# Optimization experiments

Hardware: AMD Instinct MI355X
Metric: run time of the kernel (lower is better)

## Reference

```python
import math
import jax, jax.numpy as jnp
import numpy as np

B, C, H, W = 8, 64, 128, 128
KH = KW = 3
PAD = 1
STRIDE = 1
DIL = 1
GROUPS = 4


def setup_inputs() -> dict:
    key = jax.random.key(0)
    k1, k2, k3, k4, k5 = jax.random.split(key, 5)
    x = jax.random.normal(k1, (B, C, H, W), jnp.float32)
    skip = jax.random.normal(k2, (B, C, H, W), jnp.float32)
    # offset-predicting conv: in_channels -> 2*KH*KW (has bias). Small init so offsets are modest.
    offset_w = jax.random.normal(k3, (2 * KH * KW, C, KH, KW), jnp.float32) * 0.01
    offset_b = jax.random.normal(k4, (2 * KH * KW,), jnp.float32) * 0.01
    # deformable conv weight: grouped, no bias. [Cout, Cin//G, KH, KW]
    fan_in = (C // GROUPS) * KH * KW
    deform_w = jax.random.normal(k5, (C, C // GROUPS, KH, KW), jnp.float32) * (1.0 / math.sqrt(fan_in))
    return {"x": x, "skip": skip, "offset_w": offset_w, "offset_b": offset_b, "deform_w": deform_w}


def _conv2d(x, w, b):
    y = jax.lax.conv_general_dilated(
        x, w, window_strides=(STRIDE, STRIDE), padding=((PAD, PAD), (PAD, PAD)),
        rhs_dilation=(DIL, DIL), dimension_numbers=("NCHW", "OIHW", "NCHW"))
    return y + b[None, :, None, None]


def _deform_conv(skip, offsets, w):
    # torchvision DeformConv2d semantics, offset_groups=1, zero-padded bilinear sampling.
    Bn, Cn, Hn, Wn = skip.shape
    Ho, Wo = offsets.shape[2], offsets.shape[3]
    K = KH * KW
    # offsets: [B, 2*K, Ho, Wo] ordered (k, (dy, dx))
    off = offsets.reshape(Bn, K, 2, Ho, Wo)
    off_y, off_x = off[:, :, 0], off[:, :, 1]  # [B,K,Ho,Wo]
    ky, kx = jnp.meshgrid(jnp.arange(KH), jnp.arange(KW), indexing="ij")
    ky, kx = ky.reshape(K), kx.reshape(K)
    base_y = (jnp.arange(Ho) * STRIDE - PAD)[None, None, :, None] + (ky * DIL)[None, :, None, None]
    base_x = (jnp.arange(Wo) * STRIDE - PAD)[None, None, None, :] + (kx * DIL)[None, :, None, None]
    py = base_y + off_y  # [B,K,Ho,Wo] sampling rows
    px = base_x + off_x  # sampling cols
    y0f = jnp.floor(py)
    x0f = jnp.floor(px)
    wy = py - y0f
    wx = px - x0f
    y0 = y0f.astype(jnp.int32)
    x0 = x0f.astype(jnp.int32)
    skip_flat = skip.reshape(Bn, Cn, Hn * Wn)

    def gather(yi, xi):
        valid = ((yi >= 0) & (yi < Hn) & (xi >= 0) & (xi < Wn)).astype(skip.dtype)  # [B,K,Ho,Wo]
        idx = jnp.clip(yi, 0, Hn - 1) * Wn + jnp.clip(xi, 0, Wn - 1)
        v = jax.vmap(lambda f, i: f[:, i])(skip_flat, idx.reshape(Bn, -1))  # [B,C,K*Ho*Wo]
        return v.reshape(Bn, Cn, K, Ho, Wo) * valid[:, None]

    v00 = gather(y0, x0)
    v01 = gather(y0, x0 + 1)
    v10 = gather(y0 + 1, x0)
    v11 = gather(y0 + 1, x0 + 1)
    wy_b = wy[:, None]  # [B,1,K,Ho,Wo]
    wx_b = wx[:, None]
    sampled = (v00 * (1 - wy_b) * (1 - wx_b) + v01 * (1 - wy_b) * wx_b
               + v10 * wy_b * (1 - wx_b) + v11 * wy_b * wx_b)  # [B,C,K,Ho,Wo]
    # grouped contraction with the kernel weights
    G = GROUPS
    Cg = Cn // G
    Cout = w.shape[0]
    Cog = Cout // G
    sampled_g = sampled.reshape(Bn, G, Cg, K, Ho, Wo)
    w_g = w.reshape(G, Cog, Cg, K)
    out = jnp.einsum("bgckhw,gock->bgohw", sampled_g, w_g)
    return out.reshape(Bn, Cout, Ho, Wo)


def reference(x, skip, offset_w, offset_b, deform_w):
    offsets = _conv2d(x, offset_w, offset_b)
    return _deform_conv(skip, offsets, deform_w)
```

## Files before the change

### kernel.cpp

```cpp
#include <hip/hip_runtime.h>
#include <hip/hip_fp16.h>

#define Bn    8
#define Cn    64
#define Hn    128
#define Wn    128
#define KK    9
#define OffC  18
#define NG    4
#define Cg    16
#define HW    (Hn*Wn)

#define OFFS_ELEMS (Bn*OffC*HW)
#define WAO_ELEMS  (KK*4*64*8)
#define WAD_ELEMS  (NG*KK*64*8)

#define ROWS  4
#define TR    8
#define NW    8
#define TSTR  132
#define TILE_W (NW*TR*TSTR)
#define TILE_PAD (TSTR + 4)

typedef __attribute__((ext_vector_type(8)))  short short8v;
typedef __attribute__((ext_vector_type(8)))  _Float16 half8v;
typedef __attribute__((ext_vector_type(4)))  unsigned int uint4v;
typedef __attribute__((ext_vector_type(16))) float f32x16;

__device__ __forceinline__ unsigned int rne16(float f) {
    unsigned int u = __float_as_uint(f);
    return (u + 0x7FFFu + ((u >> 16) & 1u)) >> 16;
}
__device__ __forceinline__ unsigned int pack2(float lo, float hi) {
    const unsigned int a = rne16(lo);
    unsigned int b = __float_as_uint(hi);
    b = (b + 0x7FFFu + ((b >> 16) & 1u)) & 0xFFFF0000u;
    return b | a;
}

__global__ __launch_bounds__(256) void prep_w_kernel(
    const float* __restrict__ offw, const float* __restrict__ dw,
    unsigned short* __restrict__ wAo, unsigned short* __restrict__ wAd)
{
    const int tid = blockIdx.x * 256 + threadIdx.x;
    const int nth = gridDim.x * 256;
    for (int i = tid; i < WAO_ELEMS; i += nth) {
        const int e    = i & 7;
        const int lane = (i >> 3) & 63;
        const int q    = (i >> 9) & 3;
        const int t    = i >> 11;
        const int o    = lane & 31;
        const int c    = q * 16 + 8 * (lane >> 5) + e;
        const float v  = (o < OffC) ? offw[(o * Cn + c) * KK + t] : 0.f;
        wAo[i] = (unsigned short)rne16(v);
    }
    for (int i = tid; i < WAD_ELEMS; i += nth) {
        const int e    = i & 7;
        const int lane = (i >> 3) & 63;
        const int t    = (i >> 9) % KK;
        const int g    = i / (512 * KK);
        const int o    = lane & 31;
        const int c    = 8 * (lane >> 5) + e;
        const float v  = (o < Cg) ? dw[((g * Cg + o) * Cg + c) * KK + t] : 0.f;
        wAd[i] = __half_as_ushort(__float2half_rn(v));
    }
}

__global__ __launch_bounds__(256, 4) void offset_conv_kernel(
    const float* __restrict__ x, const unsigned short* __restrict__ wAo,
    const float* __restrict__ bias, float2* __restrict__ offs2)
{
    const int tid  = threadIdx.x;
    const int wv   = tid >> 6;
    const int lane = tid & 63;
    const int p    = lane & 31;
    const int h    = lane >> 5;
    const int b    = blockIdx.y;
    const int r    = blockIdx.x;
    const int col  = wv * 32 + p;

    const float* xb = x + (size_t)b * Cn * HW;

    f32x16 acc;
#pragma unroll
    for (int i = 0; i < 16; ++i) acc[i] = 0.f;

#pragma unroll 1
    for (int q = 0; q < 4; ++q) {
        unsigned int win[4][3][3];
#pragma unroll
        for (int i = 0; i < 4; ++i) {
            const float* xc0 = xb + (size_t)(q * 16 + 8 * h + 2 * i) * HW;
            const float* xc1 = xc0 + HW;
#pragma unroll
            for (int ky = 0; ky < 3; ++ky) {
                const int  y   = r - 1 + ky;
                const bool yok = ((unsigned)y < (unsigned)Hn);
#pragma unroll
                for (int kx = 0; kx < 3; ++kx) {
                    const int  xx = col - 1 + kx;
                    const bool ok = yok && ((unsigned)xx < (unsigned)Wn);
                    const float f0 = ok ? xc0[y * Wn + xx] : 0.f;
                    const float f1 = ok ? xc1[y * Wn + xx] : 0.f;
                    win[i][ky][kx] = pack2(f0, f1);
                }
            }
        }
#pragma unroll
        for (int t = 0; t < KK; ++t) {
            uint4v bw;
            bw[0] = win[0][t / 3][t % 3];
            bw[1] = win[1][t / 3][t % 3];
            bw[2] = win[2][t / 3][t % 3];
            bw[3] = win[3][t / 3][t % 3];
            const short8v bfrag = __builtin_bit_cast(short8v, bw);
            const short8v afrag = *(const short8v*)(wAo + (size_t)(t * 4 + q) * 512 + lane * 8);
            acc = __builtin_amdgcn_mfma_f32_32x32x16_bf16(afrag, bfrag, acc, 0, 0, 0);
        }
    }

    float2* ob2 = offs2 + ((size_t)b * KK) * HW + r * Wn + col;
#pragma unroll
    for (int reg = 0; reg < 16; reg += 2) {
        const int o = (reg & 3) + 8 * (reg >> 2) + 4 * h;
        if (o < OffC) {
            const int t = o >> 1;
            float2 v;
            v.x = acc[reg]     + bias[o];
            v.y = acc[reg + 1] + bias[o + 1];
            ob2[(size_t)t * HW] = v;
        }
    }
}

struct TapS {
    int   base;
    int   gr0, gr1, gc0, gc1;
    float m00, m01, m10, m11;
    bool  cond;
};

__device__ __forceinline__ TapS tap_setup(
    int r, int col, int ky, int kx, float offy, float offx, int ylo, int yhi)
{
    TapS s;
    const float pyf = (float)(r - 1 + ky) + offy;
    const float pxf = (float)(col - 1 + kx) + offx;
    const float y0f = floorf(pyf), x0f = floorf(pxf);
    const float wy = pyf - y0f, wx = pxf - x0f;
    const int y0 = (int)y0f, x0 = (int)x0f;
    const int by = min(max(y0, 0), Hn - 1);
    const int bx = min(max(x0, 0), Wn - 1);
    const float w0p = (by == y0) ? (1.f - wy) : ((by == y0 + 1) ? wy : 0.f);
    const float w1p = (by == y0 && y0 + 1 <= Hn - 1) ? wy : 0.f;
    const float v0p = (bx == x0) ? (1.f - wx) : ((bx == x0 + 1) ? wx : 0.f);
    const float v1p = (bx == x0 && x0 + 1 <= Wn - 1) ? wx : 0.f;
    s.m00 = w0p * v0p; s.m01 = w0p * v1p;
    s.m10 = w1p * v0p; s.m11 = w1p * v1p;
    s.base = (by - ylo) * TSTR + bx;
    s.cond = (by >= ylo) && (min(by + 1, Hn - 1) <= yhi);
    s.gr0 = by; s.gr1 = min(by + 1, Hn - 1);
    s.gc0 = bx; s.gc1 = min(bx + 1, Wn - 1);
    return s;
}

__device__ __forceinline__ uint4v tap_sample(
    const TapS& s, int h, const __half2* __restrict__ tile,
    const float* __restrict__ sg)
{
    uint4v bw;
    if (s.cond) {
        const __half2 m00h = __float2half2_rn(s.m00);
        const __half2 m01h = __float2half2_rn(s.m01);
        const __half2 m10h = __float2half2_rn(s.m10);
        const __half2 m11h = __float2half2_rn(s.m11);
#pragma unroll
        for (int wi = 0; wi < 4; ++wi) {
            const __half2* tw = tile + ((4 * h + wi) * TR) * TSTR;
            __half2 a = __hmul2(tw[s.base], m00h);
            a = __hfma2(tw[s.base + 1], m01h, a);
            a = __hfma2(tw[s.base + TSTR], m10h, a);
            a = __hfma2(tw[s.base + TSTR + 1], m11h, a);
            bw[wi] = __builtin_bit_cast(unsigned int, a);
        }
    } else {
        const int ia0 = s.gr0 * Wn + s.gc0, ia1 = s.gr0 * Wn + s.gc1;
        const int ia2 = s.gr1 * Wn + s.gc0, ia3 = s.gr1 * Wn + s.gc1;
#pragma unroll
        for (int wi = 0; wi < 4; ++wi) {
            const float* sc0 = sg + (size_t)(8 * h + 2 * wi) * HW;
            const float* sc1 = sc0 + HW;
            const float v0 = sc0[ia0] * s.m00 + sc0[ia1] * s.m01 + sc0[ia2] * s.m10 + sc0[ia3] * s.m11;
            const float v1 = sc1[ia0] * s.m00 + sc1[ia1] * s.m01 + sc1[ia2] * s.m10 + sc1[ia3] * s.m11;
            bw[wi] = __builtin_bit_cast(unsigned int, __floats2half2_rn(v0, v1));
        }
    }
    return bw;
}

__device__ __forceinline__ uint4v chunk_tap(
    int r, int col, int ky, int kx, float oy, float ox, int ylo, int yhi, int h,
    const __half2* __restrict__ tile, const float* __restrict__ sg)
{
    const float pyf = (float)(r - 1 + ky) + oy;
    const float pxf = (float)(col - 1 + kx) + ox;
    const float y0f = floorf(pyf), x0f = floorf(pxf);
    const float wy = pyf - y0f, wx = pxf - x0f;
    const int y0 = (int)y0f, x0 = (int)x0f;
    const bool interior = (y0 >= ylo) & (y0 + 1 <= yhi) & (x0 >= 0) & (x0 + 1 <= Wn - 1);

    uint4v bw;
    if (__all(interior)) {
        const float iy = 1.f - wy, ix = 1.f - wx;
        const __half2 m00h = __float2half2_rn(iy * ix);
        const __half2 m01h = __float2half2_rn(iy * wx);
        const __half2 m10h = __float2half2_rn(wy * ix);
        const __half2 m11h = __float2half2_rn(wy * wx);
        const int base = (y0 - ylo) * TSTR + x0;
#pragma unroll
        for (int wi = 0; wi < 4; ++wi) {
            const __half2* tw = tile + ((4 * h + wi) * TR) * TSTR;
            __half2 a = __hmul2(tw[base], m00h);
            a = __hfma2(tw[base + 1], m01h, a);
            a = __hfma2(tw[base + TSTR], m10h, a);
            a = __hfma2(tw[base + TSTR + 1], m11h, a);
            bw[wi] = __builtin_bit_cast(unsigned int, a);
        }
    } else {
        const TapS s = tap_setup(r, col, ky, kx, oy, ox, ylo, yhi);
        bw = tap_sample(s, h, tile, sg);
    }
    return bw;
}

__global__ __launch_bounds__(512, 4) void deform_kernel(
    const float* __restrict__ skip, const float2* __restrict__ offs2,
    const unsigned short* __restrict__ wA, float* __restrict__ out)
{
    __shared__ __half2 tile[TILE_W + TILE_PAD];

    const int tid = threadIdx.x;
    const int g = blockIdx.y & 3;
    const int b = blockIdx.y >> 2;
    const int r0  = blockIdx.x * ROWS;
    const int ylo = max(0, r0 - 2);
    const int yhi = min(Hn - 1, r0 + ROWS + 1);

    const float* sg = skip + (size_t)(b * Cn + g * Cg) * HW;

    for (int i = tid; i < TILE_W; i += 512) {
        const int w  = i / (TR * TSTR);
        const int re = i % (TR * TSTR);
        const int ty = re / TSTR;
        const int xx = re % TSTR;
        const int y  = ylo + ty;
        __half2 v = __floats2half2_rn(0.f, 0.f);
        if (xx < Wn && y <= yhi) {
            const float f0 = sg[(2 * w)     * HW + y * Wn + xx];
            const float f1 = sg[(2 * w + 1) * HW + y * Wn + xx];
            v = __floats2half2_rn(f0, f1);
        }
        tile[i] = v;
    }
    for (int i = TILE_W + tid; i < TILE_W + TILE_PAD; i += 512)
        tile[i] = __floats2half2_rn(0.f, 0.f);
    __syncthreads();

    const int wv   = tid >> 6;
    const int lane = tid & 63;
    const int p    = lane & 31;
    const int h    = lane >> 5;
    const int r    = r0 + (wv >> 1);
    const int jb   = (wv & 1) * 2;
    const int colA = jb * 32 + p;
    const int colB = colA + 32;

    const unsigned short* wAg = wA + (size_t)g * (KK * 512) + lane * 8;
    const float2* offpA = offs2 + (size_t)b * KK * HW + r * Wn + colA;
    const float2* offpB = offpA + 32;

    f32x16 accA, accB;
#pragma unroll
    for (int i = 0; i < 16; ++i) { accA[i] = 0.f; accB[i] = 0.f; }

#pragma unroll
    for (int t = 0; t < KK; ++t) {
        const int ky = t / 3, kx = t % 3;
        const float2 oA = offpA[(size_t)t * HW];
        const float2 oB = offpB[(size_t)t * HW];

        const uint4v bwA = chunk_tap(r, colA, ky, kx, oA.x, oA.y, ylo, yhi, h, tile, sg);
        const uint4v bwB = chunk_tap(r, colB, ky, kx, oB.x, oB.y, ylo, yhi, h, tile, sg);

        const half8v afrag = *(const half8v*)(wAg + t * 512);
        accA = __builtin_amdgcn_mfma_f32_32x32x16_f16(afrag, __builtin_bit_cast(half8v, bwA), accA, 0, 0, 0);
        accB = __builtin_amdgcn_mfma_f32_32x32x16_f16(afrag, __builtin_bit_cast(half8v, bwB), accB, 0, 0, 0);
    }

    float* obA = out + (size_t)(b * Cn + g * Cg) * HW + r * Wn + colA;
#pragma unroll
    for (int reg = 0; reg < 8; ++reg) {
        const int o = (reg & 3) + 8 * (reg >> 2) + 4 * h;
        obA[o * HW]      = accA[reg];
        obA[o * HW + 32] = accB[reg];
    }
}

extern "C" void kernel_launch(void* const* d_in, const int* in_sizes, int n_in,
                              void* d_out, int out_size, void* d_ws, size_t ws_size,
                              hipStream_t stream) {
    const float* x        = (const float*)d_in[0];
    const float* skip     = (const float*)d_in[1];
    const float* offset_w = (const float*)d_in[2];
    const float* offset_b = (const float*)d_in[3];
    const float* deform_w = (const float*)d_in[4];
    float* out  = (float*)d_out;

    float2* offs2 = (float2*)d_ws;
    unsigned short* wAo = (unsigned short*)((float*)d_ws + OFFS_ELEMS);
    unsigned short* wAd = wAo + WAO_ELEMS;

    hipLaunchKernelGGL(prep_w_kernel, dim3(8), dim3(256), 0, stream,
                       offset_w, deform_w, wAo, wAd);
    hipLaunchKernelGGL(offset_conv_kernel, dim3(Hn, Bn), dim3(256), 0, stream,
                       x, wAo, offset_b, offs2);
    hipLaunchKernelGGL(deform_kernel, dim3(Hn / ROWS, Bn * NG), dim3(512), 0, stream,
                       skip, offs2, wAd, out);
}
```

Measured before the change: 75.78 us.

## Split deform conv tile into half-width column blocks with halo

Splits each block's work along the width into two 64-column halves. Each block now stages a 68-column tile with a halo instead of the full 128-wide row, and runs 256 threads instead of 512. The number of blocks doubles and shared memory per block roughly halves, which should raise occupancy and reduce tile-load latency. In exchange the halo columns are loaded twice, and the global-memory fallback path triggers more often near the column seams when offsets reach outside the narrower tile.

```diff
diff --git a/kernel.cpp b/kernel.cpp
--- a/kernel.cpp
+++ b/kernel.cpp
@@ -17,10 +17,11 @@
 
 #define ROWS  4
 #define TR    8
-#define NW    8
-#define TSTR  132
-#define TILE_W (NW*TR*TSTR)
-#define TILE_PAD (TSTR + 4)
+#define XT    68
+#define TSTRX 70
+#define PLANE (TR*TSTRX)
+#define TILE_WX (8*PLANE)
+#define TILE_PADX 72
 
 typedef __attribute__((ext_vector_type(8)))  short short8v;
 typedef __attribute__((ext_vector_type(8)))  _Float16 half8v;
@@ -141,7 +142,8 @@
 };
 
 __device__ __forceinline__ TapS tap_setup(
-    int r, int col, int ky, int kx, float offy, float offx, int ylo, int yhi)
+    int r, int col, int ky, int kx, float offy, float offx,
+    int ylo, int yhi, int xlo0, int xloR, int xhiR)
 {
     TapS s;
     const float pyf = (float)(r - 1 + ky) + offy;
@@ -157,8 +159,9 @@
     const float v1p = (bx == x0 && x0 + 1 <= Wn - 1) ? wx : 0.f;
     s.m00 = w0p * v0p; s.m01 = w0p * v1p;
     s.m10 = w1p * v0p; s.m11 = w1p * v1p;
-    s.base = (by - ylo) * TSTR + bx;
-    s.cond = (by >= ylo) && (min(by + 1, Hn - 1) <= yhi);
+    s.base = (by - ylo) * TSTRX + (bx - xlo0);
+    s.cond = (by >= ylo) && (min(by + 1, Hn - 1) <= yhi)
+          && (bx >= xloR) && (min(bx + 1, Wn - 1) <= xhiR);
     s.gr0 = by; s.gr1 = min(by + 1, Hn - 1);
     s.gc0 = bx; s.gc1 = min(bx + 1, Wn - 1);
     return s;
@@ -176,11 +179,11 @@
         const __half2 m11h = __float2half2_rn(s.m11);
 #pragma unroll
         for (int wi = 0; wi < 4; ++wi) {
-            const __half2* tw = tile + ((4 * h + wi) * TR) * TSTR;
+            const __half2* tw = tile + (4 * h + wi) * PLANE;
             __half2 a = __hmul2(tw[s.base], m00h);
             a = __hfma2(tw[s.base + 1], m01h, a);
-            a = __hfma2(tw[s.base + TSTR], m10h, a);
-            a = __hfma2(tw[s.base + TSTR + 1], m11h, a);
+            a = __hfma2(tw[s.base + TSTRX], m10h, a);
+            a = __hfma2(tw[s.base + TSTRX + 1], m11h, a);
             bw[wi] = __builtin_bit_cast(unsigned int, a);
         }
     } else {
@@ -199,7 +202,8 @@
 }
 
 __device__ __forceinline__ uint4v chunk_tap(
-    int r, int col, int ky, int kx, float oy, float ox, int ylo, int yhi, int h,
+    int r, int col, int ky, int kx, float oy, float ox,
+    int ylo, int yhi, int xlo0, int xloR, int xhiR, int h,
     const __half2* __restrict__ tile, const float* __restrict__ sg)
 {
     const float pyf = (float)(r - 1 + ky) + oy;
@@ -207,7 +211,7 @@
     const float y0f = floorf(pyf), x0f = floorf(pxf);
     const float wy = pyf - y0f, wx = pxf - x0f;
     const int y0 = (int)y0f, x0 = (int)x0f;
-    const bool interior = (y0 >= ylo) & (y0 + 1 <= yhi) & (x0 >= 0) & (x0 + 1 <= Wn - 1);
+    const bool interior = (y0 >= ylo) & (y0 + 1 <= yhi) & (x0 >= xloR) & (x0 + 1 <= xhiR);
 
     uint4v bw;
     if (__all(interior)) {
@@ -216,53 +220,60 @@
         const __half2 m01h = __float2half2_rn(iy * wx);
         const __half2 m10h = __float2half2_rn(wy * ix);
         const __half2 m11h = __float2half2_rn(wy * wx);
-        const int base = (y0 - ylo) * TSTR + x0;
+        const int base = (y0 - ylo) * TSTRX + (x0 - xlo0);
 #pragma unroll
         for (int wi = 0; wi < 4; ++wi) {
-            const __half2* tw = tile + ((4 * h + wi) * TR) * TSTR;
+            const __half2* tw = tile + (4 * h + wi) * PLANE;
             __half2 a = __hmul2(tw[base], m00h);
             a = __hfma2(tw[base + 1], m01h, a);
-            a = __hfma2(tw[base + TSTR], m10h, a);
-            a = __hfma2(tw[base + TSTR + 1], m11h, a);
+            a = __hfma2(tw[base + TSTRX], m10h, a);
+            a = __hfma2(tw[base + TSTRX + 1], m11h, a);
             bw[wi] = __builtin_bit_cast(unsigned int, a);
         }
     } else {
-        const TapS s = tap_setup(r, col, ky, kx, oy, ox, ylo, yhi);
+        const TapS s = tap_setup(r, col, ky, kx, oy, ox, ylo, yhi, xlo0, xloR, xhiR);
         bw = tap_sample(s, h, tile, sg);
     }
     return bw;
 }
 
-__global__ __launch_bounds__(512, 4) void deform_kernel(
+__global__ __launch_bounds__(256, 8) void deform_kernel(
     const float* __restrict__ skip, const float2* __restrict__ offs2,
     const unsigned short* __restrict__ wA, float* __restrict__ out)
 {
-    __shared__ __half2 tile[TILE_W + TILE_PAD];
+    __shared__ __half2 tile[TILE_WX + TILE_PADX];
 
     const int tid = threadIdx.x;
-    const int g = blockIdx.y & 3;
-    const int b = blockIdx.y >> 2;
+    const int yb  = blockIdx.y;
+    const int xh  = yb & 1;
+    const int g   = (yb >> 1) & 3;
+    const int b   = yb >> 3;
     const int r0  = blockIdx.x * ROWS;
     const int ylo = max(0, r0 - 2);
     const int yhi = min(Hn - 1, r0 + ROWS + 1);
+    const int xb  = xh * 64;
+    const int xlo0 = xb - 2;
+    const int xloR = max(0, xlo0);
+    const int xhiR = min(Wn - 1, xb + 65);
 
     const float* sg = skip + (size_t)(b * Cn + g * Cg) * HW;
 
-    for (int i = tid; i < TILE_W; i += 512) {
-        const int w  = i / (TR * TSTR);
-        const int re = i % (TR * TSTR);
-        const int ty = re / TSTR;
-        const int xx = re % TSTR;
+    for (int i = tid; i < TILE_WX; i += 256) {
+        const int w  = i / PLANE;
+        const int re = i % PLANE;
+        const int ty = re / TSTRX;
+        const int j  = re % TSTRX;
         const int y  = ylo + ty;
+        const int x  = xlo0 + j;
         __half2 v = __floats2half2_rn(0.f, 0.f);
-        if (xx < Wn && y <= yhi) {
-            const float f0 = sg[(2 * w)     * HW + y * Wn + xx];
-            const float f1 = sg[(2 * w + 1) * HW + y * Wn + xx];
+        if (j < XT && y <= yhi && x >= 0 && x < Wn) {
+            const float f0 = sg[(2 * w)     * HW + y * Wn + x];
+            const float f1 = sg[(2 * w + 1) * HW + y * Wn + x];
             v = __floats2half2_rn(f0, f1);
         }
         tile[i] = v;
     }
-    for (int i = TILE_W + tid; i < TILE_W + TILE_PAD; i += 512)
+    for (int i = TILE_WX + tid; i < TILE_WX + TILE_PADX; i += 256)
         tile[i] = __floats2half2_rn(0.f, 0.f);
     __syncthreads();
 
@@ -270,9 +281,8 @@
     const int lane = tid & 63;
     const int p    = lane & 31;
     const int h    = lane >> 5;
-    const int r    = r0 + (wv >> 1);
-    const int jb   = (wv & 1) * 2;
-    const int colA = jb * 32 + p;
+    const int r    = r0 + wv;
+    const int colA = xb + p;
     const int colB = colA + 32;
 
     const unsigned short* wAg = wA + (size_t)g * (KK * 512) + lane * 8;
@@ -289,8 +299,10 @@
         const float2 oA = offpA[(size_t)t * HW];
         const float2 oB = offpB[(size_t)t * HW];
 
-        const uint4v bwA = chunk_tap(r, colA, ky, kx, oA.x, oA.y, ylo, yhi, h, tile, sg);
-        const uint4v bwB = chunk_tap(r, colB, ky, kx, oB.x, oB.y, ylo, yhi, h, tile, sg);
+        const uint4v bwA = chunk_tap(r, colA, ky, kx, oA.x, oA.y,
+                                     ylo, yhi, xlo0, xloR, xhiR, h, tile, sg);
+        const uint4v bwB = chunk_tap(r, colB, ky, kx, oB.x, oB.y,
+                                     ylo, yhi, xlo0, xloR, xhiR, h, tile, sg);
 
         const half8v afrag = *(const half8v*)(wAg + t * 512);
         accA = __builtin_amdgcn_mfma_f32_32x32x16_f16(afrag, __builtin_bit_cast(half8v, bwA), accA, 0, 0, 0);
@@ -324,6 +336,6 @@
                        offset_w, deform_w, wAo, wAd);
     hipLaunchKernelGGL(offset_conv_kernel, dim3(Hn, Bn), dim3(256), 0, stream,
                        x, wAo, offset_b, offs2);
-    hipLaunchKernelGGL(deform_kernel, dim3(Hn / ROWS, Bn * NG), dim3(512), 0, stream,
+    hipLaunchKernelGGL(deform_kernel, dim3(Hn / ROWS, Bn * NG * 2), dim3(256), 0, stream,
                        skip, offs2, wAd, out);
 }
```

Measured after the change: 131.0 us. +72.9%, slower.
